# Kernel optimization log

Hardware: AMD Instinct MI355X
Metric: run time of the kernel (lower is better)

The kernel has to match this reference:

```python
import jax, jax.numpy as jnp
import numpy as np

# SSD Detect post-processing constants (match init_kwargs)
NUM_CLASSES = 21
TOP_K = 200
CONF_THRESH = 0.95
NMS_THRESH = 0.45
M_CAND = 600      # candidate cap; chosen so all boxes passing CONF_THRESH fit (~437 expected)
NEG = -1e30


def setup_inputs() -> dict:
    key = jax.random.key(0)
    k1, k2, k3 = jax.random.split(key, 3)
    B, P, C = 8, 8732, NUM_CLASSES
    loc_data = jax.random.normal(k1, (B, P, 4), dtype=jnp.float32)
    conf_data = jax.random.uniform(k2, (B, P, C), dtype=jnp.float32)
    prior_data = jax.random.uniform(k3, (1, P, 4), dtype=jnp.float32)
    return {"loc_data": loc_data, "conf_data": conf_data, "prior_data": prior_data}


def _nms_lane(boxes_all, scores):
    """One (batch, class) lane. boxes_all: [P,4], scores: [P]. Returns [TOP_K, 5]."""
    pass_mask = scores > CONF_THRESH                       # [P]
    masked = jnp.where(pass_mask, scores, jnp.float32(NEG))
    vals, idx = jax.lax.top_k(masked, M_CAND)              # score-desc candidates (prior idx)
    valid = vals > jnp.float32(NEG / 2)                    # passed threshold
    cb = boxes_all[idx]                                    # [M,4] (x1,y1,x2,y2)
    x1, y1, x2, y2 = cb[:, 0], cb[:, 1], cb[:, 2], cb[:, 3]
    area = (x2 - x1) * (y2 - y1)                           # torchvision-style, no clamp
    xx1 = jnp.maximum(x1[:, None], x1[None, :])
    yy1 = jnp.maximum(y1[:, None], y1[None, :])
    xx2 = jnp.minimum(x2[:, None], x2[None, :])
    yy2 = jnp.minimum(y2[:, None], y2[None, :])
    inter = jnp.clip(xx2 - xx1, 0.0) * jnp.clip(yy2 - yy1, 0.0)
    iou = inter / (area[:, None] + area[None, :] - inter)  # [M,M]
    ar = jnp.arange(M_CAND)

    def body(i, supp):
        keep_i = valid[i] & jnp.logical_not(supp[i])
        return supp | (keep_i & (iou[i] > NMS_THRESH) & (ar > i))

    supp = jax.lax.fori_loop(0, M_CAND, body, jnp.zeros((M_CAND,), bool))
    keep = valid & jnp.logical_not(supp)
    order = jnp.argsort(jnp.logical_not(keep))             # stable: kept first, score order
    n = jnp.minimum(keep.sum(), TOP_K)                     # number of kept boxes (<= TOP_K)
    sel_prior = idx[order[:TOP_K]]                         # prior ids of kept (score order)
    slot_valid = jnp.arange(TOP_K) < n
    fp = jnp.argmax(pass_mask)                             # first prior passing threshold
    prior_ids = jnp.where(slot_valid, sel_prior, fp)       # pad with boxes[0] like torch
    out_scores = jnp.where(slot_valid, scores[prior_ids], 0.0)
    out = jnp.concatenate([out_scores[:, None], boxes_all[prior_ids]], axis=1)  # [K,5]
    return jnp.where(pass_mask.any(), out, jnp.zeros_like(out))


def _forward(loc_data, conf_data, prior_data):
    # prior_data is accepted per the torch signature but unused by the forward math.
    per_batch = jax.vmap(
        lambda boxes, conf_b: jax.vmap(lambda s: _nms_lane(boxes, s))(conf_b[:, 1:].T)
    )
    out_fg = per_batch(loc_data, conf_data)                # [B, C-1, K, 5]
    bg = jnp.zeros_like(out_fg[:, :1])                     # background class row stays 0
    return jnp.concatenate([bg, out_fg], axis=1)           # [B, C, K, 5]


def reference(loc_data, conf_data, prior_data):
    return _forward(loc_data, conf_data, prior_data)
```

## Files before the change

kernel.cpp:

```cpp
#include <hip/hip_runtime.h>
#include <float.h>
#include <math.h>


#define P_PRIORS  8732
#define C_CLASSES 21
#define B_BATCH   8
#define NLANES    160
#define TOPK      200
#define MCAND     600
#define CONF_T    0.95f
#define NMS_T     0.45f
#define NCHUNK    64
#define CHP       137
#define CAPC      64
#define NB        64
#define MINB      0x3F733334u

#define WS_CNT2_OFF  0
#define WS_KEY2_OFF  65536
#define WS_NEED      (WS_KEY2_OFF + (size_t)NLANES * NCHUNK * CAPC * 8)

__device__ __forceinline__ uint64_t pack_key(float sc, int p) {
    return ((uint64_t)__float_as_uint(sc) << 32) | (uint32_t)(~(uint32_t)p);
}
__device__ __forceinline__ int bucket_of(uint64_t key) {
    unsigned d = (unsigned)(key >> 32) - MINB;
    int b = (int)(d >> 14);
    return b < (NB - 1) ? b : (NB - 1);
}

__global__ __launch_bounds__(256) void compact_kernel(
    const float* __restrict__ conf, unsigned char* __restrict__ ws)
{
    int*      cnts2 = (int*)(ws + WS_CNT2_OFF);
    uint64_t* keys2 = (uint64_t*)(ws + WS_KEY2_OFF);

    const int bid   = blockIdx.x;
    const int b     = bid >> 6;
    const int chunk = bid & (NCHUNK - 1);
    const int p0    = chunk * CHP;
    const int np    = min(CHP, P_PRIORS - p0);
    const int ne    = np * C_CLASSES;
    const int tid   = threadIdx.x;

    __shared__ int s_cur[20];
    if (tid < 20) s_cur[tid] = 0;
    __syncthreads();

    const float* src = conf + ((size_t)b * P_PRIORS + p0) * C_CLASSES;
    for (int t = tid; t < ne; t += 256) {
        float sc = src[t];
        if (sc > CONF_T) {
            int c = t % C_CLASSES;
            if (c != 0) {
                int p    = p0 + t / C_CLASSES;
                int slot = atomicAdd(&s_cur[c - 1], 1);
                if (slot < CAPC) {
                    int lane = b * 20 + (c - 1);
                    keys2[(((size_t)lane * NCHUNK) + chunk) * CAPC + slot] = pack_key(sc, p);
                }
            }
        }
    }
    __syncthreads();
    if (tid < 20) {
        int lane = b * 20 + tid;
        cnts2[lane * NCHUNK + chunk] = min(s_cur[tid], CAPC);
    }
}

#define IOU_ROW(BI, AI, MW, DIAG) do {                                   \
    float xx1 = fmaxf((BI).x, bj.x);                                     \
    float yy1 = fmaxf((BI).y, bj.y);                                     \
    float xx2 = fminf((BI).z, bj.z);                                     \
    float yy2 = fminf((BI).w, bj.w);                                     \
    float ww  = fmaxf(xx2 - xx1, 0.0f);                                  \
    float hh  = fmaxf(yy2 - yy1, 0.0f);                                  \
    float inter = ww * hh;                                               \
    float den   = ((AI) + aj) - inter;              \
    float iou   = inter / den;               \
    uint64_t m = __ballot(iou > NMS_T);                                  \
    if (k == c) m &= (DIAG);                                             \
    (MW) = (lid == k) ? m : (MW);                                        \
} while (0)

__device__ __forceinline__ void iou_chunk(
    int c, int wid, int lid, int M, int kmax,
    const float4* s_jb, const float* s_area, uint64_t* s_bm)
{
    const int i0 = (c << 6) + wid;
    const float4 b0 = s_jb[i0],      b1 = s_jb[i0 + 16],
                 b2 = s_jb[i0 + 32], b3 = s_jb[i0 + 48];
    const float  a0 = s_area[i0],      a1 = s_area[i0 + 16],
                 a2 = s_area[i0 + 32], a3 = s_area[i0 + 48];
    const uint64_t d0 = ~0ull << (wid + 1);
    const uint64_t d1 = ~0ull << (wid + 17);
    const uint64_t d2 = ~0ull << (wid + 33);
    const uint64_t d3 = (wid == 15) ? 0ull : (~0ull << (wid + 49));
    uint64_t w0 = 0, w1 = 0, w2 = 0, w3 = 0;
    for (int k = c; k < kmax; ++k) {
        const float4 bj = s_jb[(k << 6) + lid];
        const float  aj = s_area[(k << 6) + lid];
        IOU_ROW(b0, a0, w0, d0);
        IOU_ROW(b1, a1, w1, d1);
        IOU_ROW(b2, a2, w2, d2);
        IOU_ROW(b3, a3, w3, d3);
    }
    if (lid >= c && lid < kmax) {
        if (i0      < M) s_bm[(size_t)(i0     ) * 10 + lid] = w0;
        if (i0 + 16 < M) s_bm[(size_t)(i0 + 16) * 10 + lid] = w1;
        if (i0 + 32 < M) s_bm[(size_t)(i0 + 32) * 10 + lid] = w2;
        if (i0 + 48 < M) s_bm[(size_t)(i0 + 48) * 10 + lid] = w3;
    }
}

__global__ __launch_bounds__(1024) void fused_kernel(
    const float* __restrict__ loc, const unsigned char* __restrict__ ws,
    float* __restrict__ out)
{
    const int blane = blockIdx.x;
    const int b     = blane / C_CLASSES;
    const int cls   = blane % C_CLASSES;
    const int tid   = threadIdx.x;
    float* o = out + (size_t)blane * TOPK * 5;

    if (cls == 0) {
        for (int k = tid; k < TOPK * 5; k += 1024) o[k] = 0.0f;
        return;
    }
    const int lane = b * 20 + (cls - 1);
    const int* cnts2       = (const int*)(ws + WS_CNT2_OFF);
    const uint64_t* keys2l = (const uint64_t*)(ws + WS_KEY2_OFF)
                             + (size_t)lane * NCHUNK * CAPC;
    const float4* loc4 = (const float4*)(loc + (size_t)b * P_PRIORS * 4);

    __shared__ uint64_t s_bm[MCAND * 10];
    __shared__ float4   s_jb[640];
    __shared__ float    s_area[640];
    __shared__ float    s_ssc[MCAND];
    __shared__ int      s_ccnt[64];
    __shared__ int      s_cpre[65];
    __shared__ int      s_bcnt[NB], s_bcur[NB], s_boff[NB];
    __shared__ unsigned s_fpu;
    __shared__ uint64_t s_suppw[10], s_keepw[10];
    __shared__ int      s_prefix[10], s_n, s_mstop, s_done;

    if (tid < 64)  s_ccnt[tid] = cnts2[lane * NCHUNK + tid];
    if (tid >= 64 && tid < 128)  s_bcnt[tid - 64] = 0;
    if (tid >= 128 && tid < 192) s_bcur[tid - 128] = 0;
    if (tid == 192) s_fpu = 0xFFFFFFFFu;
    __syncthreads();
    if (tid < 64) {
        int incl = s_ccnt[tid];
        #pragma unroll
        for (int d = 1; d < 64; d <<= 1) {
            int u = __shfl_up(incl, d, 64);
            if (tid >= d) incl += u;
        }
        s_cpre[tid + 1] = incl;
        if (tid == 0) s_cpre[0] = 0;
    }
    __syncthreads();
    int cnt = s_cpre[64]; if (cnt > 1024) cnt = 1024;
    if (cnt == 0) {
        for (int k = tid; k < TOPK * 5; k += 1024) o[k] = 0.0f;
        return;
    }

    uint64_t* s_k   = s_bm;
    uint64_t* s_g   = s_bm + 1024;
    uint64_t* s_srt = s_bm + 2048;

    {
        const int wid = tid >> 6, lid = tid & 63;
        for (int c = wid; c < NCHUNK; c += 16) {
            int n_c  = s_ccnt[c];
            int base = s_cpre[c];
            if (lid < n_c) {
                int dst = base + lid;
                if (dst < 1024) s_k[dst] = keys2l[c * CAPC + lid];
            }
        }
    }
    __syncthreads();

    {
        unsigned loc_max = 0;
        for (int t = tid; t < cnt; t += 1024) {
            uint64_t kt = s_k[t];
            atomicAdd(&s_bcnt[bucket_of(kt)], 1);
            unsigned lo = (unsigned)kt;
            loc_max = lo > loc_max ? lo : loc_max;
        }
        #pragma unroll
        for (int d = 1; d < 64; d <<= 1) {
            unsigned u = (unsigned)__shfl_xor((int)loc_max, d, 64);
            loc_max = u > loc_max ? u : loc_max;
        }
        if ((tid & 63) == 0 && loc_max != 0)
            atomicMin(&s_fpu, ~loc_max);
    }
    __syncthreads();

    if (tid < 64) {
        int c = s_bcnt[63 - tid];
        int incl = c;
        #pragma unroll
        for (int d = 1; d < 64; d <<= 1) {
            int u = __shfl_up(incl, d, 64);
            if (tid >= d) incl += u;
        }
        s_boff[63 - tid] = incl - c;
    }
    __syncthreads();

    for (int t = tid; t < cnt; t += 1024) {
        uint64_t kt = s_k[t];
        int bb = bucket_of(kt);
        s_g[s_boff[bb] + atomicAdd(&s_bcur[bb], 1)] = kt;
    }
    __syncthreads();

    const int M = cnt < MCAND ? cnt : MCAND;
    {
        const int wid = tid >> 6, lid = tid & 63;
        for (int bb = wid; bb < NB; bb += 16) {
            int st = s_boff[bb], n = s_bcnt[bb];
            for (int e = lid; e < n; e += 64) {
                uint64_t kq = s_g[st + e];
                int r = st;
                for (int q = 0; q < n; ++q)
                    r += (s_g[st + q] > kq) ? 1 : 0;
                if (r < MCAND) s_srt[r] = kq;
            }
        }
    }
    __syncthreads();

    for (int i = tid; i < M; i += 1024) {
        uint64_t key = s_srt[i];
        int p = (int)(~(uint32_t)key);
        s_ssc[i]  = __uint_as_float((uint32_t)(key >> 32));
        float4 bx = loc4[p];
        s_jb[i]   = bx;
        s_area[i] = (bx.z - bx.x) * (bx.w - bx.y);
    }
    for (int i = M + tid; i < 640; i += 1024) {
        s_jb[i]   = make_float4(INFINITY, INFINITY, INFINITY, INFINITY);
        s_area[i] = INFINITY;
    }
    const int fp = (int)s_fpu;
    __syncthreads();

    const int kmax = (M + 63) >> 6;

    {
        const int wid = tid >> 6, lid = tid & 63;
        const int w   = (lid < 10) ? lid : 0;
        uint64_t supp = 0;
        int kept = 0, mstop = M;
        const int nch = kmax;

        iou_chunk(0, wid, lid, M, kmax, s_jb, s_area, s_bm);
        __syncthreads();

        for (int c = 0; c < nch; ++c) {
            if (wid == 0) {
                const int ibeg = c << 6;
                const int iend = min(ibeg + 64, M);
                uint64_t rb[8];
                #pragma unroll
                for (int d = 0; d < 8; ++d) {
                    int i = ibeg + d;
                    rb[d] = (i < iend) ? s_bm[(size_t)i * 10 + w] : 0;
                }
                for (int i = ibeg; i < iend; ++i) {
                    uint64_t row = rb[i & 7];
                    if (w < c) row = 0;
                    int ip = i + 8;
                    rb[i & 7] = (ip < iend) ? s_bm[(size_t)ip * 10 + w] : 0;
                    bool mybit = (w == c) && ((supp >> (i & 63)) & 1ull);
                    if (!__any((int)mybit)) {
                        supp |= row;
                        if (++kept == TOPK) { mstop = i + 1; break; }
                    }
                }
                if (lid == 0) s_done = (kept >= TOPK) ? 1 : 0;
                if (kept < TOPK && c + 1 < nch)
                    iou_chunk(c + 1, 0, lid, M, kmax, s_jb, s_area, s_bm);
            } else if (c + 1 < nch) {
                iou_chunk(c + 1, wid, lid, M, kmax, s_jb, s_area, s_bm);
            }
            __syncthreads();
            if (s_done) break;
        }
        if (wid == 0) {
            if (lid < 10) s_suppw[lid] = supp;
            if (lid == 0) s_mstop = mstop;
        }
    }
    __syncthreads();

    if (tid == 0) {
        const int Me = s_mstop;
        int total = 0;
        for (int w = 0; w < 10; ++w) {
            uint64_t kw = 0;
            int rem = Me - (w << 6);
            if (rem > 0) {
                uint64_t vm = (rem >= 64) ? ~0ull : ((1ull << rem) - 1ull);
                kw = (~s_suppw[w]) & vm;
            }
            s_keepw[w]  = kw;
            s_prefix[w] = total;
            total += __popcll(kw);
        }
        s_n = total < TOPK ? total : TOPK;
    }
    __syncthreads();

    const int n  = s_n;
    const int Me = s_mstop;
    float4 fbox = loc4[fp];
    for (int k = tid; k < TOPK; k += 1024) {
        if (k >= n) {
            o[k * 5 + 0] = 0.0f;
            o[k * 5 + 1] = fbox.x; o[k * 5 + 2] = fbox.y;
            o[k * 5 + 3] = fbox.z; o[k * 5 + 4] = fbox.w;
        }
    }
    for (int t = tid; t < Me; t += 1024) {
        uint64_t kw = s_keepw[t >> 6];
        if ((kw >> (t & 63)) & 1ull) {
            int r = s_prefix[t >> 6] + __popcll(kw & ((1ull << (t & 63)) - 1ull));
            if (r < TOPK) {
                float4 bx = s_jb[t];
                o[r * 5 + 0] = s_ssc[t];
                o[r * 5 + 1] = bx.x; o[r * 5 + 2] = bx.y;
                o[r * 5 + 3] = bx.z; o[r * 5 + 4] = bx.w;
            }
        }
    }
}

__global__ __launch_bounds__(512) void detect_fallback(
    const float* __restrict__ loc, const float* __restrict__ conf,
    float* __restrict__ out)
{
    const int lane = blockIdx.x;
    const int b    = lane / C_CLASSES;
    const int cls  = lane % C_CLASSES;
    const int tid  = threadIdx.x;
    float* o = out + (size_t)lane * TOPK * 5;
    if (cls == 0) { for (int k = tid; k < TOPK * 5; k += 512) o[k] = 0.0f; return; }

    __shared__ uint64_t s_buf[MCAND * 10];
    __shared__ float4   s_box[MCAND + 40];
    __shared__ float    s_score[MCAND + 40];
    __shared__ uint64_t s_suppw[10];
    __shared__ uint64_t s_keepw[10];
    __shared__ int      s_prefix[10];
    __shared__ int      s_count, s_fp, s_n;

    if (tid == 0) { s_count = 0; s_fp = 0x7FFFFFFF; }
    __syncthreads();
    const float* confb = conf + (size_t)b * P_PRIORS * C_CLASSES + cls;
    const float* locb  = loc  + (size_t)b * P_PRIORS * 4;
    for (int p = tid; p < P_PRIORS; p += 512) {
        float sc = confb[(size_t)p * C_CLASSES];
        if (sc > CONF_T) {
            int pos = atomicAdd(&s_count, 1);
            if (pos < 1024) s_buf[pos] = pack_key(sc, p);
            atomicMin(&s_fp, p);
        }
    }
    __syncthreads();
    int cnt = s_count; if (cnt > 1024) cnt = 1024;
    if (cnt == 0) { for (int k = tid; k < TOPK * 5; k += 512) o[k] = 0.0f; return; }
    uint64_t* s_sorted = s_buf + 1024;
    if (tid < cnt) {
        uint64_t kt = s_buf[tid];
        int r = 0;
        for (int j = 0; j < cnt; ++j) r += (s_buf[j] > kt) ? 1 : 0;
        if (r < MCAND) s_sorted[r] = kt;
    }
    __syncthreads();
    const int M = cnt < MCAND ? cnt : MCAND;
    const int kmax = (M + 63) >> 6;
    for (int i = tid; i < M; i += 512) {
        uint64_t key = s_sorted[i];
        int p = (int)(~(uint32_t)key);
        s_score[i] = __uint_as_float((uint32_t)(key >> 32));
        s_box[i]   = ((const float4*)locb)[p];
    }
    __syncthreads();
    {
        const int wid = tid >> 6, lid = tid & 63;
        for (int i = wid; i < M; i += 8) {
            float4 bi = s_box[i];
            float  ai = (bi.z - bi.x) * (bi.w - bi.y);
            for (int k = i >> 6; k < kmax; ++k) {
                int j = (k << 6) + lid;
                float4 bj = s_box[j];
                float  aj = (bj.z - bj.x) * (bj.w - bj.y);
                float inter = fmaxf(fminf(bi.z, bj.z) - fmaxf(bi.x, bj.x), 0.0f)
                            * fmaxf(fminf(bi.w, bj.w) - fmaxf(bi.y, bj.y), 0.0f);
                float iou = inter / ((ai + aj) - inter);
                uint64_t m = __ballot((iou > NMS_T) & (j > i) & (j < M));
                if (lid == 0) s_buf[i * 10 + k] = m;
            }
        }
    }
    __syncthreads();
    if (tid < 64) {
        const int w = (tid < 10) ? tid : 0;
        uint64_t rb[8];
        #pragma unroll
        for (int d = 0; d < 8; ++d) rb[d] = (d < M) ? s_buf[d * 10 + w] : 0;
        uint64_t supp = 0;
        for (int i0 = 0; i0 < M; i0 += 8) {
            #pragma unroll
            for (int d = 0; d < 8; ++d) {
                int i = i0 + d;
                if (i < M) {
                    uint64_t row = rb[d];
                    if (w < (i >> 6)) row = 0;
                    int ip = i + 8;
                    rb[d] = (ip < M) ? s_buf[ip * 10 + w] : 0;
                    unsigned part  = (unsigned)(supp >> (i & 32));
                    unsigned wordv = (unsigned)__builtin_amdgcn_readlane((int)part, i >> 6);
                    if (!((wordv >> (i & 31)) & 1u)) supp |= row;
                }
            }
        }
        if (tid < 10) s_suppw[tid] = supp;
    }
    __syncthreads();
    if (tid == 0) {
        int total = 0;
        for (int w = 0; w < 10; ++w) {
            uint64_t kw = 0;
            if (w < kmax) {
                int rem = M - (w << 6);
                uint64_t vm = (rem >= 64) ? ~0ull : ((1ull << rem) - 1ull);
                kw = (~s_suppw[w]) & vm;
            }
            s_keepw[w] = kw; s_prefix[w] = total; total += __popcll(kw);
        }
        s_n = total < TOPK ? total : TOPK;
    }
    __syncthreads();
    const int n = s_n, fp = s_fp;
    float4 fbox = ((const float4*)locb)[fp];
    for (int k = tid; k < TOPK; k += 512) {
        if (k >= n) {
            o[k * 5 + 0] = 0.0f;
            o[k * 5 + 1] = fbox.x; o[k * 5 + 2] = fbox.y;
            o[k * 5 + 3] = fbox.z; o[k * 5 + 4] = fbox.w;
        }
    }
    for (int t = tid; t < M; t += 512) {
        uint64_t kw = s_keepw[t >> 6];
        if ((kw >> (t & 63)) & 1ull) {
            int r = s_prefix[t >> 6] + __popcll(kw & ((1ull << (t & 63)) - 1ull));
            if (r < TOPK) {
                float4 bx = s_box[t];
                o[r * 5 + 0] = s_score[t];
                o[r * 5 + 1] = bx.x; o[r * 5 + 2] = bx.y;
                o[r * 5 + 3] = bx.z; o[r * 5 + 4] = bx.w;
            }
        }
    }
}

extern "C" void kernel_launch(void* const* d_in, const int* in_sizes, int n_in,
                              void* d_out, int out_size, void* d_ws, size_t ws_size,
                              hipStream_t stream) {
    const float* loc  = (const float*)d_in[0];
    const float* conf = (const float*)d_in[1];
    float* out = (float*)d_out;
    unsigned char* ws = (unsigned char*)d_ws;

    if (ws_size >= WS_NEED) {
        compact_kernel<<<dim3(B_BATCH * NCHUNK),    dim3(256),  0, stream>>>(conf, ws);
        fused_kernel  <<<dim3(B_BATCH * C_CLASSES), dim3(1024), 0, stream>>>(loc, ws, out);
    } else {
        detect_fallback<<<dim3(B_BATCH * C_CLASSES), dim3(512), 0, stream>>>(loc, conf, out);
    }
}
```

Measured before the change: 113.1 us.

## Fuse compaction into single per-lane kernel with wave-aggregated atomics

Removes the separate compaction kernel and its workspace round-trip. Each (batch, class) block now scans its own strided conf column directly, appending passing keys via wave ballot with one shared atomic per wave, and tracks the first passing prior with atomicMin. Block-to-lane mapping is changed so consecutive blocks share a class, which may help L2 locality. The cost is strided 84-byte-stride reads per lane (each conf line read 20 times across blocks) in exchange for saving a launch and global key traffic.

Measured after the change: 109.0 us. 3.6% less time.

```diff
diff --git a/kernel.cpp b/kernel.cpp
--- a/kernel.cpp
+++ b/kernel.cpp
@@ -6,20 +6,12 @@
 #define P_PRIORS  8732
 #define C_CLASSES 21
 #define B_BATCH   8
-#define NLANES    160
 #define TOPK      200
 #define MCAND     600
 #define CONF_T    0.95f
 #define NMS_T     0.45f
-#define NCHUNK    64
-#define CHP       137
-#define CAPC      64
 #define NB        64
 #define MINB      0x3F733334u
-
-#define WS_CNT2_OFF  0
-#define WS_KEY2_OFF  65536
-#define WS_NEED      (WS_KEY2_OFF + (size_t)NLANES * NCHUNK * CAPC * 8)
 
 __device__ __forceinline__ uint64_t pack_key(float sc, int p) {
     return ((uint64_t)__float_as_uint(sc) << 32) | (uint32_t)(~(uint32_t)p);
@@ -28,46 +20,6 @@
     unsigned d = (unsigned)(key >> 32) - MINB;
     int b = (int)(d >> 14);
     return b < (NB - 1) ? b : (NB - 1);
-}
-
-__global__ __launch_bounds__(256) void compact_kernel(
-    const float* __restrict__ conf, unsigned char* __restrict__ ws)
-{
-    int*      cnts2 = (int*)(ws + WS_CNT2_OFF);
-    uint64_t* keys2 = (uint64_t*)(ws + WS_KEY2_OFF);
-
-    const int bid   = blockIdx.x;
-    const int b     = bid >> 6;
-    const int chunk = bid & (NCHUNK - 1);
-    const int p0    = chunk * CHP;
-    const int np    = min(CHP, P_PRIORS - p0);
-    const int ne    = np * C_CLASSES;
-    const int tid   = threadIdx.x;
-
-    __shared__ int s_cur[20];
-    if (tid < 20) s_cur[tid] = 0;
-    __syncthreads();
-
-    const float* src = conf + ((size_t)b * P_PRIORS + p0) * C_CLASSES;
-    for (int t = tid; t < ne; t += 256) {
-        float sc = src[t];
-        if (sc > CONF_T) {
-            int c = t % C_CLASSES;
-            if (c != 0) {
-                int p    = p0 + t / C_CLASSES;
-                int slot = atomicAdd(&s_cur[c - 1], 1);
-                if (slot < CAPC) {
-                    int lane = b * 20 + (c - 1);
-                    keys2[(((size_t)lane * NCHUNK) + chunk) * CAPC + slot] = pack_key(sc, p);
-                }
-            }
-        }
-    }
-    __syncthreads();
-    if (tid < 20) {
-        int lane = b * 20 + tid;
-        cnts2[lane * NCHUNK + chunk] = min(s_cur[tid], CAPC);
-    }
 }
 
 #define IOU_ROW(BI, AI, MW, DIAG) do {                                   \
@@ -115,92 +67,71 @@
     }
 }
 
-__global__ __launch_bounds__(1024) void fused_kernel(
-    const float* __restrict__ loc, const unsigned char* __restrict__ ws,
+__global__ __launch_bounds__(1024) void detect_one(
+    const float* __restrict__ loc, const float* __restrict__ conf,
     float* __restrict__ out)
 {
-    const int blane = blockIdx.x;
-    const int b     = blane / C_CLASSES;
-    const int cls   = blane % C_CLASSES;
-    const int tid   = threadIdx.x;
-    float* o = out + (size_t)blane * TOPK * 5;
+    const int b   = blockIdx.x & 7;
+    const int cls = blockIdx.x >> 3;
+    const int tid = threadIdx.x;
+    float* o = out + ((size_t)(b * C_CLASSES + cls)) * TOPK * 5;
 
     if (cls == 0) {
         for (int k = tid; k < TOPK * 5; k += 1024) o[k] = 0.0f;
         return;
     }
-    const int lane = b * 20 + (cls - 1);
-    const int* cnts2       = (const int*)(ws + WS_CNT2_OFF);
-    const uint64_t* keys2l = (const uint64_t*)(ws + WS_KEY2_OFF)
-                             + (size_t)lane * NCHUNK * CAPC;
-    const float4* loc4 = (const float4*)(loc + (size_t)b * P_PRIORS * 4);
+
+    const float*  confb = conf + (size_t)b * P_PRIORS * C_CLASSES + cls;
+    const float4* loc4  = (const float4*)(loc + (size_t)b * P_PRIORS * 4);
 
     __shared__ uint64_t s_bm[MCAND * 10];
     __shared__ float4   s_jb[640];
     __shared__ float    s_area[640];
     __shared__ float    s_ssc[MCAND];
-    __shared__ int      s_ccnt[64];
-    __shared__ int      s_cpre[65];
     __shared__ int      s_bcnt[NB], s_bcur[NB], s_boff[NB];
-    __shared__ unsigned s_fpu;
+    __shared__ int      s_cnt, s_fp;
     __shared__ uint64_t s_suppw[10], s_keepw[10];
     __shared__ int      s_prefix[10], s_n, s_mstop, s_done;
 
-    if (tid < 64)  s_ccnt[tid] = cnts2[lane * NCHUNK + tid];
-    if (tid >= 64 && tid < 128)  s_bcnt[tid - 64] = 0;
-    if (tid >= 128 && tid < 192) s_bcur[tid - 128] = 0;
-    if (tid == 192) s_fpu = 0xFFFFFFFFu;
-    __syncthreads();
-    if (tid < 64) {
-        int incl = s_ccnt[tid];
-        #pragma unroll
-        for (int d = 1; d < 64; d <<= 1) {
-            int u = __shfl_up(incl, d, 64);
-            if (tid >= d) incl += u;
-        }
-        s_cpre[tid + 1] = incl;
-        if (tid == 0) s_cpre[0] = 0;
-    }
-    __syncthreads();
-    int cnt = s_cpre[64]; if (cnt > 1024) cnt = 1024;
+    uint64_t* s_k   = s_bm;
+    uint64_t* s_g   = s_bm + 1024;
+    uint64_t* s_srt = s_bm + 2048;
+
+    if (tid < NB)                    s_bcnt[tid] = 0;
+    else if (tid < 2 * NB)           s_bcur[tid - NB] = 0;
+    else if (tid == 2 * NB)        { s_cnt = 0; s_fp = 0x7FFFFFFF; }
+    __syncthreads();
+
+    {
+        const int lid = tid & 63;
+        for (int p = tid; p < P_PRIORS; p += 1024) {
+            float sc = confb[(size_t)p * C_CLASSES];
+            bool pass = sc > CONF_T;
+            uint64_t mask = __ballot(pass);
+            if (mask != 0) {
+                int leader = (int)__ffsll((unsigned long long)mask) - 1;
+                int base = 0;
+                if (lid == leader) {
+                    base = atomicAdd(&s_cnt, __popcll(mask));
+                    atomicMin(&s_fp, p);
+                }
+                base = __shfl(base, leader, 64);
+                if (pass) {
+                    int pos = base + __popcll(mask & ((1ull << lid) - 1ull));
+                    if (pos < 1024) s_k[pos] = pack_key(sc, p);
+                }
+            }
+        }
+    }
+    __syncthreads();
+    int cnt = s_cnt; if (cnt > 1024) cnt = 1024;
     if (cnt == 0) {
         for (int k = tid; k < TOPK * 5; k += 1024) o[k] = 0.0f;
         return;
     }
 
-    uint64_t* s_k   = s_bm;
-    uint64_t* s_g   = s_bm + 1024;
-    uint64_t* s_srt = s_bm + 2048;
-
-    {
-        const int wid = tid >> 6, lid = tid & 63;
-        for (int c = wid; c < NCHUNK; c += 16) {
-            int n_c  = s_ccnt[c];
-            int base = s_cpre[c];
-            if (lid < n_c) {
-                int dst = base + lid;
-                if (dst < 1024) s_k[dst] = keys2l[c * CAPC + lid];
-            }
-        }
-    }
-    __syncthreads();
-
-    {
-        unsigned loc_max = 0;
-        for (int t = tid; t < cnt; t += 1024) {
-            uint64_t kt = s_k[t];
-            atomicAdd(&s_bcnt[bucket_of(kt)], 1);
-            unsigned lo = (unsigned)kt;
-            loc_max = lo > loc_max ? lo : loc_max;
-        }
-        #pragma unroll
-        for (int d = 1; d < 64; d <<= 1) {
-            unsigned u = (unsigned)__shfl_xor((int)loc_max, d, 64);
-            loc_max = u > loc_max ? u : loc_max;
-        }
-        if ((tid & 63) == 0 && loc_max != 0)
-            atomicMin(&s_fpu, ~loc_max);
-    }
+    for (int t = tid; t < cnt; t += 1024)
+        atomicAdd(&s_bcnt[bucket_of(s_k[t])], 1);
     __syncthreads();
 
     if (tid < 64) {
@@ -250,7 +181,7 @@
         s_jb[i]   = make_float4(INFINITY, INFINITY, INFINITY, INFINITY);
         s_area[i] = INFINITY;
     }
-    const int fp = (int)s_fpu;
+    const int fp = s_fp;
     __syncthreads();
 
     const int kmax = (M + 63) >> 6;
@@ -344,148 +275,13 @@
     }
 }
 
-__global__ __launch_bounds__(512) void detect_fallback(
-    const float* __restrict__ loc, const float* __restrict__ conf,
-    float* __restrict__ out)
-{
-    const int lane = blockIdx.x;
-    const int b    = lane / C_CLASSES;
-    const int cls  = lane % C_CLASSES;
-    const int tid  = threadIdx.x;
-    float* o = out + (size_t)lane * TOPK * 5;
-    if (cls == 0) { for (int k = tid; k < TOPK * 5; k += 512) o[k] = 0.0f; return; }
-
-    __shared__ uint64_t s_buf[MCAND * 10];
-    __shared__ float4   s_box[MCAND + 40];
-    __shared__ float    s_score[MCAND + 40];
-    __shared__ uint64_t s_suppw[10];
-    __shared__ uint64_t s_keepw[10];
-    __shared__ int      s_prefix[10];
-    __shared__ int      s_count, s_fp, s_n;
-
-    if (tid == 0) { s_count = 0; s_fp = 0x7FFFFFFF; }
-    __syncthreads();
-    const float* confb = conf + (size_t)b * P_PRIORS * C_CLASSES + cls;
-    const float* locb  = loc  + (size_t)b * P_PRIORS * 4;
-    for (int p = tid; p < P_PRIORS; p += 512) {
-        float sc = confb[(size_t)p * C_CLASSES];
-        if (sc > CONF_T) {
-            int pos = atomicAdd(&s_count, 1);
-            if (pos < 1024) s_buf[pos] = pack_key(sc, p);
-            atomicMin(&s_fp, p);
-        }
-    }
-    __syncthreads();
-    int cnt = s_count; if (cnt > 1024) cnt = 1024;
-    if (cnt == 0) { for (int k = tid; k < TOPK * 5; k += 512) o[k] = 0.0f; return; }
-    uint64_t* s_sorted = s_buf + 1024;
-    if (tid < cnt) {
-        uint64_t kt = s_buf[tid];
-        int r = 0;
-        for (int j = 0; j < cnt; ++j) r += (s_buf[j] > kt) ? 1 : 0;
-        if (r < MCAND) s_sorted[r] = kt;
-    }
-    __syncthreads();
-    const int M = cnt < MCAND ? cnt : MCAND;
-    const int kmax = (M + 63) >> 6;
-    for (int i = tid; i < M; i += 512) {
-        uint64_t key = s_sorted[i];
-        int p = (int)(~(uint32_t)key);
-        s_score[i] = __uint_as_float((uint32_t)(key >> 32));
-        s_box[i]   = ((const float4*)locb)[p];
-    }
-    __syncthreads();
-    {
-        const int wid = tid >> 6, lid = tid & 63;
-        for (int i = wid; i < M; i += 8) {
-            float4 bi = s_box[i];
-            float  ai = (bi.z - bi.x) * (bi.w - bi.y);
-            for (int k = i >> 6; k < kmax; ++k) {
-                int j = (k << 6) + lid;
-                float4 bj = s_box[j];
-                float  aj = (bj.z - bj.x) * (bj.w - bj.y);
-                float inter = fmaxf(fminf(bi.z, bj.z) - fmaxf(bi.x, bj.x), 0.0f)
-                            * fmaxf(fminf(bi.w, bj.w) - fmaxf(bi.y, bj.y), 0.0f);
-                float iou = inter / ((ai + aj) - inter);
-                uint64_t m = __ballot((iou > NMS_T) & (j > i) & (j < M));
-                if (lid == 0) s_buf[i * 10 + k] = m;
-            }
-        }
-    }
-    __syncthreads();
-    if (tid < 64) {
-        const int w = (tid < 10) ? tid : 0;
-        uint64_t rb[8];
-        #pragma unroll
-        for (int d = 0; d < 8; ++d) rb[d] = (d < M) ? s_buf[d * 10 + w] : 0;
-        uint64_t supp = 0;
-        for (int i0 = 0; i0 < M; i0 += 8) {
-            #pragma unroll
-            for (int d = 0; d < 8; ++d) {
-                int i = i0 + d;
-                if (i < M) {
-                    uint64_t row = rb[d];
-                    if (w < (i >> 6)) row = 0;
-                    int ip = i + 8;
-                    rb[d] = (ip < M) ? s_buf[ip * 10 + w] : 0;
-                    unsigned part  = (unsigned)(supp >> (i & 32));
-                    unsigned wordv = (unsigned)__builtin_amdgcn_readlane((int)part, i >> 6);
-                    if (!((wordv >> (i & 31)) & 1u)) supp |= row;
-                }
-            }
-        }
-        if (tid < 10) s_suppw[tid] = supp;
-    }
-    __syncthreads();
-    if (tid == 0) {
-        int total = 0;
-        for (int w = 0; w < 10; ++w) {
-            uint64_t kw = 0;
-            if (w < kmax) {
-                int rem = M - (w << 6);
-                uint64_t vm = (rem >= 64) ? ~0ull : ((1ull << rem) - 1ull);
-                kw = (~s_suppw[w]) & vm;
-            }
-            s_keepw[w] = kw; s_prefix[w] = total; total += __popcll(kw);
-        }
-        s_n = total < TOPK ? total : TOPK;
-    }
-    __syncthreads();
-    const int n = s_n, fp = s_fp;
-    float4 fbox = ((const float4*)locb)[fp];
-    for (int k = tid; k < TOPK; k += 512) {
-        if (k >= n) {
-            o[k * 5 + 0] = 0.0f;
-            o[k * 5 + 1] = fbox.x; o[k * 5 + 2] = fbox.y;
-            o[k * 5 + 3] = fbox.z; o[k * 5 + 4] = fbox.w;
-        }
-    }
-    for (int t = tid; t < M; t += 512) {
-        uint64_t kw = s_keepw[t >> 6];
-        if ((kw >> (t & 63)) & 1ull) {
-            int r = s_prefix[t >> 6] + __popcll(kw & ((1ull << (t & 63)) - 1ull));
-            if (r < TOPK) {
-                float4 bx = s_box[t];
-                o[r * 5 + 0] = s_score[t];
-                o[r * 5 + 1] = bx.x; o[r * 5 + 2] = bx.y;
-                o[r * 5 + 3] = bx.z; o[r * 5 + 4] = bx.w;
-            }
-        }
-    }
-}
-
 extern "C" void kernel_launch(void* const* d_in, const int* in_sizes, int n_in,
                               void* d_out, int out_size, void* d_ws, size_t ws_size,
                               hipStream_t stream) {
     const float* loc  = (const float*)d_in[0];
     const float* conf = (const float*)d_in[1];
     float* out = (float*)d_out;
-    unsigned char* ws = (unsigned char*)d_ws;
-
-    if (ws_size >= WS_NEED) {
-        compact_kernel<<<dim3(B_BATCH * NCHUNK),    dim3(256),  0, stream>>>(conf, ws);
-        fused_kernel  <<<dim3(B_BATCH * C_CLASSES), dim3(1024), 0, stream>>>(loc, ws, out);
-    } else {
-        detect_fallback<<<dim3(B_BATCH * C_CLASSES), dim3(512), 0, stream>>>(loc, conf, out);
-    }
-}
+    (void)d_ws; (void)ws_size;
+
+    detect_one<<<dim3(B_BATCH * C_CLASSES), dim3(1024), 0, stream>>>(loc, conf, out);
+}
```
